# Kernel tuning notes

Measured on AMD Instinct MI355X. Metric: run time of the kernel, lower is better.

The kernel has to match this reference:

```python
import jax, jax.numpy as jnp
import numpy as np

D_MODEL = 1024
N_HEADS = 16
TREE_DEPTH = 5
B, T = 2, 1024


def setup_inputs() -> dict:
    key = jax.random.key(0)
    k1, k2, k3, k4 = jax.random.split(key, 4)
    sc = 1.0 / np.sqrt(D_MODEL)
    return {
        "x": jax.random.normal(k1, (B, T, D_MODEL), dtype=jnp.float32),
        "Wp": jax.random.normal(k2, (D_MODEL, N_HEADS * TREE_DEPTH), dtype=jnp.float32) * sc,
        "bp": jnp.zeros((N_HEADS * TREE_DEPTH,), dtype=jnp.float32),
        "Wv": jax.random.normal(k3, (D_MODEL, D_MODEL), dtype=jnp.float32) * sc,
        "Wo": jax.random.normal(k4, (D_MODEL, D_MODEL), dtype=jnp.float32) * sc,
    }


def reference(x, Wp, bp, Wv, Wo):
    Bc, Tc, d = x.shape
    H, Dt = N_HEADS, TREE_DEPTH
    dh = d // H
    # tree paths: (B, H, T, Dt)
    paths = jax.nn.sigmoid(x @ Wp + bp).reshape(Bc, Tc, H, Dt).transpose(0, 2, 1, 3)
    pq = paths[:, :, :, None, :]  # (B,H,T,1,Dt)
    pk = paths[:, :, None, :, :]  # (B,H,1,T,Dt)
    agree = pq * pk + (1.0 - pq) * (1.0 - pk)  # (B,H,T,T,Dt)
    sim = jnp.cumprod(agree, axis=-1).sum(axis=-1) / Dt  # (B,H,T,T)
    # causal mask (strict upper triangle -> -inf)
    causal_mask = jnp.triu(jnp.ones((Tc, Tc), dtype=bool), k=1)
    sim = jnp.where(causal_mask[None, None], -jnp.inf, sim)
    attn = jax.nn.softmax(sim, axis=-1)
    V = (x @ Wv).reshape(Bc, Tc, H, dh).transpose(0, 2, 1, 3)  # (B,H,T,dh)
    ctx = jnp.einsum("bhqk,bhkd->bhqd", attn, V)
    ctx = ctx.transpose(0, 2, 1, 3).reshape(Bc, Tc, d)
    return ctx @ Wo
```

## Files before the change

### kernel.cpp

```cpp
#include <hip/hip_runtime.h>
#include <hip/hip_bf16.h>

#define B_SZ 2
#define T_SEQ 1024
#define D_MODEL 1024
#define N_HEADS 16
#define TREE_DEPTH 5
#define DH 64

typedef __attribute__((ext_vector_type(8))) short short8;
typedef __attribute__((ext_vector_type(4))) float f32x4;

__device__ __forceinline__ ushort f2bf(float f) {
    uint32_t u = __float_as_uint(f);
    u += 0x7FFFu + ((u >> 16) & 1u);
    return (ushort)(u >> 16);
}

__global__ __launch_bounds__(256) void convert_bf16(
    const float* __restrict__ in, ushort* __restrict__ out)
{
    const int i = (blockIdx.x * 256 + threadIdx.x) * 8;
    const float4 a = *(const float4*)(in + i);
    const float4 b = *(const float4*)(in + i + 4);
    ushort o[8] = {f2bf(a.x), f2bf(a.y), f2bf(a.z), f2bf(a.w),
                   f2bf(b.x), f2bf(b.y), f2bf(b.z), f2bf(b.w)};
    *(uint4*)(out + i) = *(const uint4*)o;
}

__global__ __launch_bounds__(256) void transpose_bf16(
    const float* __restrict__ W, ushort* __restrict__ Wt, int K, int N)
{
    __shared__ float tile[32][33];
    const int n0 = blockIdx.x * 32, k0 = blockIdx.y * 32;
    const int tx = threadIdx.x & 31, ty = threadIdx.x >> 5;
    #pragma unroll
    for (int i = 0; i < 4; ++i)
        tile[ty + i * 8][tx] = W[(size_t)(k0 + ty + i * 8) * N + n0 + tx];
    __syncthreads();
    #pragma unroll
    for (int i = 0; i < 4; ++i)
        Wt[(size_t)(n0 + ty + i * 8) * K + k0 + tx] = f2bf(tile[tx][ty + i * 8]);
}

__global__ __launch_bounds__(256) void transpose_wp(
    const float* __restrict__ Wp, ushort* __restrict__ Wpt)
{
    __shared__ float tile[64 * 80];
    const int k0 = blockIdx.x * 64;
    #pragma unroll
    for (int j = 0; j < 20; ++j) {
        const int i = threadIdx.x + j * 256;
        tile[i] = Wp[(size_t)k0 * 80 + i];
    }
    __syncthreads();
    #pragma unroll
    for (int j = 0; j < 20; ++j) {
        const int o = threadIdx.x + j * 256;
        const int n = o >> 6, k = o & 63;
        Wpt[(size_t)n * 1024 + k0 + k] = f2bf(tile[k * 80 + n]);
    }
}

__global__ __launch_bounds__(256) void paths_phi(
    const ushort* __restrict__ xb, const ushort* __restrict__ Wpt,
    const float* __restrict__ bp, ushort* __restrict__ Phi)
{
    __shared__ float red[4][16][80];
    __shared__ float p_s[16][80];
    const int tid = threadIdx.x;
    const int lane = tid & 63, w = tid >> 6;
    const int quad = lane >> 4, m16 = lane & 15;
    const int row0 = blockIdx.x * 16;

    f32x4 acc[5];
    #pragma unroll
    for (int nb = 0; nb < 5; ++nb) acc[nb] = (f32x4)0.0f;

    const ushort* ap = xb + (size_t)(row0 + m16) * 1024 + w * 256 + quad * 8;
    const ushort* bpz = Wpt + (size_t)m16 * 1024 + w * 256 + quad * 8;
    #pragma unroll
    for (int it = 0; it < 8; ++it) {
        const short8 af = *(const short8*)(ap + it * 32);
        #pragma unroll
        for (int nb = 0; nb < 5; ++nb) {
            const short8 bf = *(const short8*)(bpz + (size_t)nb * 16 * 1024 + it * 32);
            acc[nb] = __builtin_amdgcn_mfma_f32_16x16x32_bf16(af, bf, acc[nb], 0, 0, 0);
        }
    }
    #pragma unroll
    for (int nb = 0; nb < 5; ++nb)
        #pragma unroll
        for (int r = 0; r < 4; ++r)
            red[w][quad * 4 + r][nb * 16 + m16] = acc[nb][r];
    __syncthreads();
    #pragma unroll
    for (int j = 0; j < 5; ++j) {
        const int i = tid + j * 256;
        const int rr = i / 80, cc = i - rr * 80;
        const float v = red[0][rr][cc] + red[1][rr][cc] +
                        red[2][rr][cc] + red[3][rr][cc] + bp[cc];
        p_s[rr][cc] = 1.0f / (1.0f + __expf(-v));
    }
    __syncthreads();
    #pragma unroll
    for (int j = 0; j < 8; ++j) {
        const int c = tid + j * 256;
        const int rr = c >> 7, rem = c & 127;
        const int h = rem >> 3, f8 = (rem & 7) * 8;
        const float* pr = &p_s[rr][h * 5];
        ushort o[8];
        #pragma unroll
        for (int e = 0; e < 8; ++e) {
            const int f = f8 + e;
            float val = 0.0f;
            if (f < 62) {
                int d, off;
                if (f < 2)       { d = 1; off = 0; }
                else if (f < 6)  { d = 2; off = 2; }
                else if (f < 14) { d = 3; off = 6; }
                else if (f < 30) { d = 4; off = 14; }
                else             { d = 5; off = 30; }
                const int e2 = f - off;
                float prod = 1.0f;
                for (int jj = 1; jj <= d; ++jj) {
                    const float p = pr[jj - 1];
                    prod *= ((e2 >> (d - jj)) & 1) ? (1.0f - p) : p;
                }
                val = prod;
            }
            o[e] = f2bf(val);
        }
        const int grow = row0 + rr;
        const int b = grow >> 10, t = grow & 1023;
        *(uint4*)(Phi + ((size_t)(b * 16 + h) * 1024 + t) * 64 + f8) =
            *(const uint4*)o;
    }
}

template <bool OUT_BF16>
__global__ __launch_bounds__(256) void gemm_bf16(
    const ushort* __restrict__ A, const ushort* __restrict__ Bt,
    void* __restrict__ Cv, int M, int N, int K)
{
    __shared__ ushort As[128 * 32];
    __shared__ ushort Bs[64 * 32];

    const int tid = threadIdx.x;
    const int lane = tid & 63;
    const int w = tid >> 6;
    const int wm = w & 1, wn = w >> 1;
    const int rowBase = blockIdx.y * 128;
    const int colBase = blockIdx.x * 64;

    const int quad = tid & 3;
    const int arow0 = tid >> 2;
    const int brow = tid >> 2;

    const int am0 = arow0, am1 = arow0 + 64;
    const int aoff0 = (am0 >> 4) * 512 + (quad * 16 + (am0 & 15)) * 8;
    const int aoff1 = (am1 >> 4) * 512 + (quad * 16 + (am1 & 15)) * 8;
    const int boff  = (brow >> 4) * 512 + (quad * 16 + (brow & 15)) * 8;

    const ushort* Ap0 = A + (size_t)(rowBase + am0) * K + quad * 8;
    const ushort* Ap1 = A + (size_t)(rowBase + am1) * K + quad * 8;
    const ushort* Bp  = Bt + (size_t)(colBase + brow) * K + quad * 8;

    f32x4 acc[4][2];
    #pragma unroll
    for (int i = 0; i < 4; ++i) {
        acc[i][0] = (f32x4)0.0f;
        acc[i][1] = (f32x4)0.0f;
    }

    const int niter = K / 32;
    uint4 ga0 = *(const uint4*)Ap0;
    uint4 ga1 = *(const uint4*)Ap1;
    uint4 gb  = *(const uint4*)Bp;

    for (int it = 0; it < niter; ++it) {
        __syncthreads();
        *(uint4*)(As + aoff0) = ga0;
        *(uint4*)(As + aoff1) = ga1;
        *(uint4*)(Bs + boff)  = gb;
        __syncthreads();
        if (it + 1 < niter) {
            ga0 = *(const uint4*)(Ap0 + (it + 1) * 32);
            ga1 = *(const uint4*)(Ap1 + (it + 1) * 32);
            gb  = *(const uint4*)(Bp  + (it + 1) * 32);
        }
        short8 af[4], bf[2];
        #pragma unroll
        for (int j = 0; j < 4; ++j)
            af[j] = *(const short8*)(As + (wm * 4 + j) * 512 + lane * 8);
        #pragma unroll
        for (int j = 0; j < 2; ++j)
            bf[j] = *(const short8*)(Bs + (wn * 2 + j) * 512 + lane * 8);
        #pragma unroll
        for (int i = 0; i < 4; ++i)
            #pragma unroll
            for (int j = 0; j < 2; ++j)
                acc[i][j] = __builtin_amdgcn_mfma_f32_16x16x32_bf16(
                    af[i], bf[j], acc[i][j], 0, 0, 0);
    }

    const int cq = lane >> 4, cl = lane & 15;
    #pragma unroll
    for (int i = 0; i < 4; ++i)
        #pragma unroll
        for (int j = 0; j < 2; ++j) {
            const int col = colBase + wn * 32 + j * 16 + cl;
            #pragma unroll
            for (int r = 0; r < 4; ++r) {
                const int row = rowBase + wm * 64 + i * 16 + cq * 4 + r;
                if (OUT_BF16)
                    ((ushort*)Cv)[(size_t)row * N + col] = f2bf(acc[i][j][r]);
                else
                    ((float*)Cv)[(size_t)row * N + col] = acc[i][j][r];
            }
        }
}

__global__ __launch_bounds__(256) void attn_mfma(
    const ushort* __restrict__ Phi, const ushort* __restrict__ Vt,
    ushort* __restrict__ ctxb)
{
    const int qt = 15 - blockIdx.x;
    const int bh = blockIdx.y;
    const int b = bh >> 4, h = bh & 15;
    const int tid = threadIdx.x;
    const int lane = tid & 63;
    const int w = tid >> 6;
    const int quad = lane >> 4, m16 = lane & 15;

    __shared__ ushort K_s[4096];
    __shared__ ushort V_s[4096];
    __shared__ ushort W_s[4096];

    const int qrow = qt * 64 + w * 16 + m16;
    const ushort* qbase = Phi + ((size_t)bh * 1024 + qrow) * 64 + quad * 8;
    const short8 qf0 = *(const short8*)qbase;
    const short8 qf1 = *(const short8*)(qbase + 32);

    f32x4 cacc[4];
    #pragma unroll
    for (int nb = 0; nb < 4; ++nb) cacc[nb] = (f32x4)0.0f;
    float den[4] = {0.f, 0.f, 0.f, 0.f};

    const int r0 = tid >> 3;
    const int c8 = (tid & 7) * 8;
    const int ks_st = c8 >> 5, kc_st = (c8 >> 3) & 3;

    for (int kt = 0; kt <= qt; ++kt) {
        __syncthreads();
        #pragma unroll
        for (int i = 0; i < 2; ++i) {
            const int r = r0 + i * 32;
            const int dst = ((r >> 4) * 2 + ks_st) * 512 + (kc_st * 16 + (r & 15)) * 8;
            *(uint4*)(K_s + dst) =
                *(const uint4*)(Phi + ((size_t)bh * 1024 + kt * 64 + r) * 64 + c8);
            *(uint4*)(V_s + dst) =
                *(const uint4*)(Vt + (size_t)(h * 64 + r) * (B_SZ * T_SEQ) +
                                b * 1024 + kt * 64 + c8);
        }
        __syncthreads();

        #pragma unroll
        for (int nb = 0; nb < 4; ++nb) {
            const short8 kf0 = *(const short8*)(K_s + (nb * 2 + 0) * 512 + lane * 8);
            const short8 kf1 = *(const short8*)(K_s + (nb * 2 + 1) * 512 + lane * 8);
            f32x4 s = (f32x4)0.0f;
            s = __builtin_amdgcn_mfma_f32_16x16x32_bf16(qf0, kf0, s, 0, 0, 0);
            s = __builtin_amdgcn_mfma_f32_16x16x32_bf16(qf1, kf1, s, 0, 0, 0);
            const int key = nb * 16 + m16;
            const int kglob = kt * 64 + key;
            const int qg0 = qt * 64 + w * 16 + quad * 4;
            const int wbase = (w * 2 + (key >> 5)) * 512 + (((key >> 3) & 3) * 16) * 8 +
                              (quad * 4) * 8 + (key & 7);
            #pragma unroll
            for (int r = 0; r < 4; ++r) {
                float wgt = 0.0f;
                if (kglob <= qg0 + r) wgt = __expf(s[r] * 0.2f);
                den[r] += wgt;
                W_s[wbase + r * 8] = f2bf(wgt);
            }
        }
        __syncthreads();

        const short8 wf0 = *(const short8*)(W_s + (w * 2 + 0) * 512 + lane * 8);
        const short8 wf1 = *(const short8*)(W_s + (w * 2 + 1) * 512 + lane * 8);
        #pragma unroll
        for (int nb = 0; nb < 4; ++nb) {
            const short8 vf0 = *(const short8*)(V_s + (nb * 2 + 0) * 512 + lane * 8);
            const short8 vf1 = *(const short8*)(V_s + (nb * 2 + 1) * 512 + lane * 8);
            cacc[nb] = __builtin_amdgcn_mfma_f32_16x16x32_bf16(wf0, vf0, cacc[nb], 0, 0, 0);
            cacc[nb] = __builtin_amdgcn_mfma_f32_16x16x32_bf16(wf1, vf1, cacc[nb], 0, 0, 0);
        }
    }

    #pragma unroll
    for (int r = 0; r < 4; ++r) {
        den[r] += __shfl_xor(den[r], 1);
        den[r] += __shfl_xor(den[r], 2);
        den[r] += __shfl_xor(den[r], 4);
        den[r] += __shfl_xor(den[r], 8);
        den[r] = 1.0f / den[r];
    }

    #pragma unroll
    for (int nb = 0; nb < 4; ++nb) {
        const int dim = h * 64 + nb * 16 + m16;
        #pragma unroll
        for (int r = 0; r < 4; ++r) {
            const int token = qt * 64 + w * 16 + quad * 4 + r;
            ctxb[(size_t)(b * 1024 + token) * D_MODEL + dim] = f2bf(cacc[nb][r] * den[r]);
        }
    }
}

extern "C" void kernel_launch(void* const* d_in, const int* in_sizes, int n_in,
                              void* d_out, int out_size, void* d_ws, size_t ws_size,
                              hipStream_t stream)
{
    const float* x  = (const float*)d_in[0];
    const float* Wp = (const float*)d_in[1];
    const float* bp = (const float*)d_in[2];
    const float* Wv = (const float*)d_in[3];
    const float* Wo = (const float*)d_in[4];
    float* out = (float*)d_out;

    const int M = B_SZ * T_SEQ;
    char* ws = (char*)d_ws;
    ushort* xb   = (ushort*)(ws);
    ushort* Wvt  = (ushort*)(ws + (4u  << 20));
    ushort* Wot  = (ushort*)(ws + (6u  << 20));
    ushort* Phi  = (ushort*)(ws + (8u  << 20));
    ushort* Vt   = (ushort*)(ws + (12u << 20));
    ushort* ctxb = (ushort*)(ws + (16u << 20));
    ushort* Wpt  = (ushort*)(ws + (20u << 20));

    convert_bf16<<<M * D_MODEL / (256 * 8), 256, 0, stream>>>(x, xb);
    transpose_wp<<<16, 256, 0, stream>>>(Wp, Wpt);
    transpose_bf16<<<dim3(32, 32), 256, 0, stream>>>(Wv, Wvt, D_MODEL, D_MODEL);
    transpose_bf16<<<dim3(32, 32), 256, 0, stream>>>(Wo, Wot, D_MODEL, D_MODEL);
    paths_phi<<<128, 256, 0, stream>>>(xb, Wpt, bp, Phi);

    gemm_bf16<true><<<dim3(M / 64, D_MODEL / 128), 256, 0, stream>>>(
        Wvt, xb, Vt, D_MODEL, M, D_MODEL);
    attn_mfma<<<dim3(16, 32), 256, 0, stream>>>(Phi, Vt, ctxb);
    gemm_bf16<false><<<dim3(D_MODEL / 64, M / 128), 256, 0, stream>>>(
        ctxb, Wot, out, M, D_MODEL, D_MODEL);
}
```

Measured before the change: 175.6 us.

## Merge prologue and mid kernels, stage GEMM tiles with global_load_lds

Merges the bf16 conversion and the three weight transposes into one prologue launch, and runs the V projection GEMM and the paths/Phi computation as separate block ranges of a single launch. Cuts the launch count from eight to four and lets independent work share the GPU concurrently. The GEMM body now loads tiles straight into LDS with global_load_lds instead of register-staged prefetch, which removes the software double-buffer overlap of the next tile's global load with the current MFMAs.

```diff
diff --git a/kernel.cpp b/kernel.cpp
--- a/kernel.cpp
+++ b/kernel.cpp
@@ -17,61 +17,137 @@
     return (ushort)(u >> 16);
 }
 
-__global__ __launch_bounds__(256) void convert_bf16(
-    const float* __restrict__ in, ushort* __restrict__ out)
-{
-    const int i = (blockIdx.x * 256 + threadIdx.x) * 8;
-    const float4 a = *(const float4*)(in + i);
-    const float4 b = *(const float4*)(in + i + 4);
-    ushort o[8] = {f2bf(a.x), f2bf(a.y), f2bf(a.z), f2bf(a.w),
-                   f2bf(b.x), f2bf(b.y), f2bf(b.z), f2bf(b.w)};
-    *(uint4*)(out + i) = *(const uint4*)o;
-}
-
-__global__ __launch_bounds__(256) void transpose_bf16(
-    const float* __restrict__ W, ushort* __restrict__ Wt, int K, int N)
-{
-    __shared__ float tile[32][33];
-    const int n0 = blockIdx.x * 32, k0 = blockIdx.y * 32;
-    const int tx = threadIdx.x & 31, ty = threadIdx.x >> 5;
+__device__ __forceinline__ void gll16(const void* g, void* l) {
+    __builtin_amdgcn_global_load_lds(
+        (const __attribute__((address_space(1))) void*)g,
+        (__attribute__((address_space(3))) void*)l, 16, 0, 0);
+}
+
+__global__ __launch_bounds__(256) void prologue(
+    const float* __restrict__ x, const float* __restrict__ Wv,
+    const float* __restrict__ Wo, const float* __restrict__ Wp,
+    ushort* __restrict__ xb, ushort* __restrict__ Wvt,
+    ushort* __restrict__ Wot, ushort* __restrict__ Wpt)
+{
+    __shared__ __align__(16) char sm[20480];
+    const int bid = blockIdx.x, tid = threadIdx.x;
+    if (bid < 1024) {
+        const int i = (bid * 256 + tid) * 8;
+        const float4 a = *(const float4*)(x + i);
+        const float4 b = *(const float4*)(x + i + 4);
+        ushort o[8] = {f2bf(a.x), f2bf(a.y), f2bf(a.z), f2bf(a.w),
+                       f2bf(b.x), f2bf(b.y), f2bf(b.z), f2bf(b.w)};
+        *(uint4*)(xb + i) = *(const uint4*)o;
+    } else if (bid < 3072) {
+        const int t = bid - 1024;
+        const float* W = (t < 1024) ? Wv : Wo;
+        ushort* Wt = (t < 1024) ? Wvt : Wot;
+        const int ti = t & 1023;
+        const int n0 = (ti & 31) * 32, k0 = (ti >> 5) * 32;
+        float (*tile)[33] = (float(*)[33])sm;
+        const int tx = tid & 31, ty = tid >> 5;
+        #pragma unroll
+        for (int i = 0; i < 4; ++i)
+            tile[ty + i * 8][tx] = W[(size_t)(k0 + ty + i * 8) * 1024 + n0 + tx];
+        __syncthreads();
+        #pragma unroll
+        for (int i = 0; i < 4; ++i)
+            Wt[(size_t)(n0 + ty + i * 8) * 1024 + k0 + tx] = f2bf(tile[tx][ty + i * 8]);
+    } else {
+        float* tile = (float*)sm;
+        const int k0 = (bid - 3072) * 64;
+        #pragma unroll
+        for (int j = 0; j < 20; ++j) {
+            const int i = tid + j * 256;
+            tile[i] = Wp[(size_t)k0 * 80 + i];
+        }
+        __syncthreads();
+        #pragma unroll
+        for (int j = 0; j < 20; ++j) {
+            const int o = tid + j * 256;
+            const int n = o >> 6, k = o & 63;
+            Wpt[(size_t)n * 1024 + k0 + k] = f2bf(tile[k * 80 + n]);
+        }
+    }
+}
+
+template <bool OUT_BF16>
+__device__ __forceinline__ void gemm_body(
+    const ushort* __restrict__ A, const ushort* __restrict__ Bt,
+    void* __restrict__ Cv, int N, int K, int bx, int by,
+    ushort* As, ushort* Bs)
+{
+    const int tid = threadIdx.x;
+    const int lane = tid & 63;
+    const int w = tid >> 6;
+    const int wm = w & 1, wn = w >> 1;
+    const int rowBase = by * 128;
+    const int colBase = bx * 64;
+
+    const int srow = lane & 15;
+    const int sk = (lane >> 4) * 8;
+
+    const ushort* gA0 = A + (size_t)(rowBase + 2 * w * 16 + srow) * K + sk;
+    const ushort* gA1 = gA0 + (size_t)16 * K;
+    const ushort* gB  = Bt + (size_t)(colBase + w * 16 + srow) * K + sk;
+    ushort* dA0 = As + (2 * w) * 512;
+    ushort* dA1 = As + (2 * w + 1) * 512;
+    ushort* dB  = Bs + w * 512;
+
+    f32x4 acc[4][2];
+    #pragma unroll
+    for (int i = 0; i < 4; ++i) {
+        acc[i][0] = (f32x4)0.0f;
+        acc[i][1] = (f32x4)0.0f;
+    }
+
+    for (int it = 0; it < K / 32; ++it) {
+        __syncthreads();
+        gll16(gA0 + it * 32, dA0);
+        gll16(gA1 + it * 32, dA1);
+        gll16(gB  + it * 32, dB);
+        __syncthreads();
+        short8 af[4], bf[2];
+        #pragma unroll
+        for (int j = 0; j < 4; ++j)
+            af[j] = *(const short8*)(As + (wm * 4 + j) * 512 + lane * 8);
+        #pragma unroll
+        for (int j = 0; j < 2; ++j)
+            bf[j] = *(const short8*)(Bs + (wn * 2 + j) * 512 + lane * 8);
+        #pragma unroll
+        for (int i = 0; i < 4; ++i)
+            #pragma unroll
+            for (int j = 0; j < 2; ++j)
+                acc[i][j] = __builtin_amdgcn_mfma_f32_16x16x32_bf16(
+                    af[i], bf[j], acc[i][j], 0, 0, 0);
+    }
+
+    const int cq = lane >> 4, cl = lane & 15;
     #pragma unroll
     for (int i = 0; i < 4; ++i)
-        tile[ty + i * 8][tx] = W[(size_t)(k0 + ty + i * 8) * N + n0 + tx];
-    __syncthreads();
-    #pragma unroll
-    for (int i = 0; i < 4; ++i)
-        Wt[(size_t)(n0 + ty + i * 8) * K + k0 + tx] = f2bf(tile[tx][ty + i * 8]);
-}
-
-__global__ __launch_bounds__(256) void transpose_wp(
-    const float* __restrict__ Wp, ushort* __restrict__ Wpt)
-{
-    __shared__ float tile[64 * 80];
-    const int k0 = blockIdx.x * 64;
-    #pragma unroll
-    for (int j = 0; j < 20; ++j) {
-        const int i = threadIdx.x + j * 256;
-        tile[i] = Wp[(size_t)k0 * 80 + i];
-    }
-    __syncthreads();
-    #pragma unroll
-    for (int j = 0; j < 20; ++j) {
-        const int o = threadIdx.x + j * 256;
-        const int n = o >> 6, k = o & 63;
-        Wpt[(size_t)n * 1024 + k0 + k] = f2bf(tile[k * 80 + n]);
-    }
-}
-
-__global__ __launch_bounds__(256) void paths_phi(
+        #pragma unroll
+        for (int j = 0; j < 2; ++j) {
+            const int col = colBase + wn * 32 + j * 16 + cl;
+            #pragma unroll
+            for (int r = 0; r < 4; ++r) {
+                const int row = rowBase + wm * 64 + i * 16 + cq * 4 + r;
+                if (OUT_BF16)
+                    ((ushort*)Cv)[(size_t)row * N + col] = f2bf(acc[i][j][r]);
+                else
+                    ((float*)Cv)[(size_t)row * N + col] = acc[i][j][r];
+            }
+        }
+}
+
+__device__ __forceinline__ void phi_body(
     const ushort* __restrict__ xb, const ushort* __restrict__ Wpt,
-    const float* __restrict__ bp, ushort* __restrict__ Phi)
-{
-    __shared__ float red[4][16][80];
-    __shared__ float p_s[16][80];
+    const float* __restrict__ bp, ushort* __restrict__ Phi,
+    int blk, float* red, float* p_s)
+{
     const int tid = threadIdx.x;
     const int lane = tid & 63, w = tid >> 6;
     const int quad = lane >> 4, m16 = lane & 15;
-    const int row0 = blockIdx.x * 16;
+    const int row0 = blk * 16;
 
     f32x4 acc[5];
     #pragma unroll
@@ -92,15 +168,15 @@
     for (int nb = 0; nb < 5; ++nb)
         #pragma unroll
         for (int r = 0; r < 4; ++r)
-            red[w][quad * 4 + r][nb * 16 + m16] = acc[nb][r];
+            red[(w * 16 + quad * 4 + r) * 80 + nb * 16 + m16] = acc[nb][r];
     __syncthreads();
     #pragma unroll
     for (int j = 0; j < 5; ++j) {
         const int i = tid + j * 256;
         const int rr = i / 80, cc = i - rr * 80;
-        const float v = red[0][rr][cc] + red[1][rr][cc] +
-                        red[2][rr][cc] + red[3][rr][cc] + bp[cc];
-        p_s[rr][cc] = 1.0f / (1.0f + __expf(-v));
+        const float v = red[(0 * 16 + rr) * 80 + cc] + red[(1 * 16 + rr) * 80 + cc] +
+                        red[(2 * 16 + rr) * 80 + cc] + red[(3 * 16 + rr) * 80 + cc] + bp[cc];
+        p_s[rr * 80 + cc] = 1.0f / (1.0f + __expf(-v));
     }
     __syncthreads();
     #pragma unroll
@@ -108,7 +184,7 @@
         const int c = tid + j * 256;
         const int rr = c >> 7, rem = c & 127;
         const int h = rem >> 3, f8 = (rem & 7) * 8;
-        const float* pr = &p_s[rr][h * 5];
+        const float* pr = &p_s[rr * 80 + h * 5];
         ushort o[8];
         #pragma unroll
         for (int e = 0; e < 8; ++e) {
@@ -138,87 +214,31 @@
     }
 }
 
-template <bool OUT_BF16>
-__global__ __launch_bounds__(256) void gemm_bf16(
-    const ushort* __restrict__ A, const ushort* __restrict__ Bt,
-    void* __restrict__ Cv, int M, int N, int K)
-{
-    __shared__ ushort As[128 * 32];
-    __shared__ ushort Bs[64 * 32];
-
-    const int tid = threadIdx.x;
-    const int lane = tid & 63;
-    const int w = tid >> 6;
-    const int wm = w & 1, wn = w >> 1;
-    const int rowBase = blockIdx.y * 128;
-    const int colBase = blockIdx.x * 64;
-
-    const int quad = tid & 3;
-    const int arow0 = tid >> 2;
-    const int brow = tid >> 2;
-
-    const int am0 = arow0, am1 = arow0 + 64;
-    const int aoff0 = (am0 >> 4) * 512 + (quad * 16 + (am0 & 15)) * 8;
-    const int aoff1 = (am1 >> 4) * 512 + (quad * 16 + (am1 & 15)) * 8;
-    const int boff  = (brow >> 4) * 512 + (quad * 16 + (brow & 15)) * 8;
-
-    const ushort* Ap0 = A + (size_t)(rowBase + am0) * K + quad * 8;
-    const ushort* Ap1 = A + (size_t)(rowBase + am1) * K + quad * 8;
-    const ushort* Bp  = Bt + (size_t)(colBase + brow) * K + quad * 8;
-
-    f32x4 acc[4][2];
-    #pragma unroll
-    for (int i = 0; i < 4; ++i) {
-        acc[i][0] = (f32x4)0.0f;
-        acc[i][1] = (f32x4)0.0f;
-    }
-
-    const int niter = K / 32;
-    uint4 ga0 = *(const uint4*)Ap0;
-    uint4 ga1 = *(const uint4*)Ap1;
-    uint4 gb  = *(const uint4*)Bp;
-
-    for (int it = 0; it < niter; ++it) {
-        __syncthreads();
-        *(uint4*)(As + aoff0) = ga0;
-        *(uint4*)(As + aoff1) = ga1;
-        *(uint4*)(Bs + boff)  = gb;
-        __syncthreads();
-        if (it + 1 < niter) {
-            ga0 = *(const uint4*)(Ap0 + (it + 1) * 32);
-            ga1 = *(const uint4*)(Ap1 + (it + 1) * 32);
-            gb  = *(const uint4*)(Bp  + (it + 1) * 32);
-        }
-        short8 af[4], bf[2];
-        #pragma unroll
-        for (int j = 0; j < 4; ++j)
-            af[j] = *(const short8*)(As + (wm * 4 + j) * 512 + lane * 8);
-        #pragma unroll
-        for (int j = 0; j < 2; ++j)
-            bf[j] = *(const short8*)(Bs + (wn * 2 + j) * 512 + lane * 8);
-        #pragma unroll
-        for (int i = 0; i < 4; ++i)
-            #pragma unroll
-            for (int j = 0; j < 2; ++j)
-                acc[i][j] = __builtin_amdgcn_mfma_f32_16x16x32_bf16(
-                    af[i], bf[j], acc[i][j], 0, 0, 0);
-    }
-
-    const int cq = lane >> 4, cl = lane & 15;
-    #pragma unroll
-    for (int i = 0; i < 4; ++i)
-        #pragma unroll
-        for (int j = 0; j < 2; ++j) {
-            const int col = colBase + wn * 32 + j * 16 + cl;
-            #pragma unroll
-            for (int r = 0; r < 4; ++r) {
-                const int row = rowBase + wm * 64 + i * 16 + cq * 4 + r;
-                if (OUT_BF16)
-                    ((ushort*)Cv)[(size_t)row * N + col] = f2bf(acc[i][j][r]);
-                else
-                    ((float*)Cv)[(size_t)row * N + col] = acc[i][j][r];
-            }
-        }
+__global__ __launch_bounds__(256) void mid_kernel(
+    const ushort* __restrict__ xb, const ushort* __restrict__ Wvt,
+    const ushort* __restrict__ Wpt, const float* __restrict__ bp,
+    ushort* __restrict__ Vt, ushort* __restrict__ Phi)
+{
+    __shared__ __align__(16) char sm[25600];
+    if (blockIdx.x < 256) {
+        ushort* As = (ushort*)sm;
+        ushort* Bs = As + 128 * 32;
+        gemm_body<true>(Wvt, xb, Vt, 2048, 1024,
+                        blockIdx.x & 31, blockIdx.x >> 5, As, Bs);
+    } else {
+        float* red = (float*)sm;
+        float* p_s = (float*)(sm + 20480);
+        phi_body(xb, Wpt, bp, Phi, blockIdx.x - 256, red, p_s);
+    }
+}
+
+__global__ __launch_bounds__(256) void gemm_out(
+    const ushort* __restrict__ ctxb, const ushort* __restrict__ Wot,
+    float* __restrict__ out)
+{
+    __shared__ __align__(16) ushort sm[128 * 32 + 64 * 32];
+    gemm_body<false>(ctxb, Wot, out, 1024, 1024,
+                     blockIdx.x, blockIdx.y, sm, sm + 128 * 32);
 }
 
 __global__ __launch_bounds__(256) void attn_mfma(
@@ -329,7 +349,6 @@
     const float* Wo = (const float*)d_in[4];
     float* out = (float*)d_out;
 
-    const int M = B_SZ * T_SEQ;
     char* ws = (char*)d_ws;
     ushort* xb   = (ushort*)(ws);
     ushort* Wvt  = (ushort*)(ws + (4u  << 20));
@@ -339,15 +358,8 @@
     ushort* ctxb = (ushort*)(ws + (16u << 20));
     ushort* Wpt  = (ushort*)(ws + (20u << 20));
 
-    convert_bf16<<<M * D_MODEL / (256 * 8), 256, 0, stream>>>(x, xb);
-    transpose_wp<<<16, 256, 0, stream>>>(Wp, Wpt);
-    transpose_bf16<<<dim3(32, 32), 256, 0, stream>>>(Wv, Wvt, D_MODEL, D_MODEL);
-    transpose_bf16<<<dim3(32, 32), 256, 0, stream>>>(Wo, Wot, D_MODEL, D_MODEL);
-    paths_phi<<<128, 256, 0, stream>>>(xb, Wpt, bp, Phi);
-
-    gemm_bf16<true><<<dim3(M / 64, D_MODEL / 128), 256, 0, stream>>>(
-        Wvt, xb, Vt, D_MODEL, M, D_MODEL);
+    prologue<<<3088, 256, 0, stream>>>(x, Wv, Wo, Wp, xb, Wvt, Wot, Wpt);
+    mid_kernel<<<384, 256, 0, stream>>>(xb, Wvt, Wpt, bp, Vt, Phi);
     attn_mfma<<<dim3(16, 32), 256, 0, stream>>>(Phi, Vt, ctxb);
-    gemm_bf16<false><<<dim3(D_MODEL / 64, M / 128), 256, 0, stream>>>(
-        ctxb, Wot, out, M, D_MODEL, D_MODEL);
-}
+    gemm_out<<<dim3(16, 16), 256, 0, stream>>>(ctxb, Wot, out);
+}
```

After: 160.1 us. 1.1x faster.
